# Kernel optimization log

Hardware: AMD Instinct MI355X
Metric: run time of the kernel (lower is better)

## Reference

```python
import jax, jax.numpy as jnp
import numpy as np

N = 100000
E = 1600000
IN = 128
H = 4
C = 32
NEG_SLOPE = 0.2


def setup_inputs() -> dict:
    key = jax.random.key(0)
    ks = jax.random.split(key, 10)
    feats = jax.random.normal(ks[0], (N, IN), dtype=jnp.float32)
    # edge_index with no self loops: dst = (src + offset) % N, offset in [1, N-1]
    src = jax.random.randint(ks[1], (E,), 0, N)
    off = jax.random.randint(ks[2], (E,), 1, N)
    dst = (src + off) % N
    edge_index = jnp.stack([src, dst]).astype(jnp.int64)
    scale = 1.0 / np.sqrt(IN)
    W_src = jax.random.uniform(ks[3], (H * C, IN), jnp.float32, -scale, scale)
    W_res = jax.random.uniform(ks[4], (H * C, IN), jnp.float32, -scale, scale)
    att_src = jax.random.normal(ks[5], (1, H, C), dtype=jnp.float32) * 0.1
    att_dst = jax.random.normal(ks[6], (1, H, C), dtype=jnp.float32) * 0.1
    bias = jnp.zeros((H * C,), dtype=jnp.float32)
    gamma = jnp.ones((H * C,), dtype=jnp.float32)
    beta = jnp.zeros((H * C,), dtype=jnp.float32)
    return {"feats": feats, "edge_index": edge_index, "W_src": W_src,
            "att_src": att_src, "att_dst": att_dst, "W_res": W_res,
            "bias": bias, "gamma": gamma, "beta": beta}


def reference(feats, edge_index, W_src, att_src, att_dst, W_res, bias, gamma, beta):
    n = feats.shape[0]
    # add self loops (edge_index has none by construction)
    loop = jnp.arange(n)
    src = jnp.concatenate([edge_index[0], loop])  # [E+N]
    dst = jnp.concatenate([edge_index[1], loop])
    xp = (feats @ W_src.T).reshape(n, H, C)          # [N,H,C]
    a_src = jnp.sum(xp * att_src, axis=-1)           # [N,H]
    a_dst = jnp.sum(xp * att_dst, axis=-1)           # [N,H]
    e = jax.nn.leaky_relu(a_src[src] + a_dst[dst], NEG_SLOPE)  # [E+N,H]
    # segment softmax over destination node
    m = jax.ops.segment_max(e, dst, num_segments=n)
    ex = jnp.exp(e - m[dst])
    s = jax.ops.segment_sum(ex, dst, num_segments=n)
    alpha = ex / (s[dst] + 1e-16)                    # [E+N,H]
    # weighted scatter-add aggregation
    msg = alpha[:, :, None] * xp[src]                # [E+N,H,C]
    out = jax.ops.segment_sum(msg, dst, num_segments=n)  # [N,H,C]
    res = (feats @ W_res.T).reshape(n, H, C)
    out = out + res + bias.reshape(1, H, C)
    out = out.reshape(n, H * C)                      # agg_modes='flatten'
    # BatchNorm1d, training mode (batch statistics, biased variance)
    mu = out.mean(axis=0)
    var = jnp.mean((out - mu) ** 2, axis=0)
    return (out - mu) / jnp.sqrt(var + 1e-5) * gamma + beta
```

## Files before the change

### kernel.cpp

```cpp
#include <hip/hip_runtime.h>
#include <hip/hip_fp16.h>

#define NEGS 0.2f
#define NB_AGGR 2048
#define NSHAD 16
#define NB_CSR 2048
#define CAP 64

typedef _Float16 f16x8 __attribute__((ext_vector_type(8)));
typedef float f32x2 __attribute__((ext_vector_type(2)));
typedef float f32x4 __attribute__((ext_vector_type(4)));

__device__ __forceinline__ float lrelu(float x){ return x > 0.f ? x : NEGS*x; }
__device__ __forceinline__ float sel4(float4 v, int h){
    float lo = (h & 1) ? v.y : v.x;
    float hi = (h & 1) ? v.w : v.z;
    return (h & 2) ? hi : lo;
}

__device__ __forceinline__ unsigned char f32_to_e4m3(float x){
    union { _Float16 f; unsigned short u; } c; c.f = (_Float16)x;
    unsigned u = c.u, s = (u >> 8) & 0x80, a = u & 0x7fff;
    if (a < 0x2400) return (unsigned char)s;
    a += 0x40;
    unsigned e = (a >> 10) - 8;
    unsigned m = (a >> 7) & 7;
    return (unsigned char)(s | (e << 3) | m);
}
template<bool HI>
__device__ __forceinline__ float2 fp8x2_to_f2(unsigned int packed){
#if __has_builtin(__builtin_amdgcn_cvt_pk_f32_fp8)
    f32x2 r = __builtin_amdgcn_cvt_pk_f32_fp8((int)packed, HI);
    return make_float2(r[0], r[1]);
#else
    unsigned short sv = HI ? (unsigned short)(packed >> 16) : (unsigned short)(packed & 0xffff);
    unsigned b0 = sv & 0xff, b1 = (sv >> 8) & 0xff;
    unsigned t0 = b0 & 0x7f, t1 = b1 & 0x7f;
    unsigned short u0 = (unsigned short)(((b0 & 0x80) << 8) | (t0 ? ((t0 + 64) << 7) : 0));
    unsigned short u1 = (unsigned short)(((b1 & 0x80) << 8) | (t1 ? ((t1 + 64) << 7) : 0));
    union { unsigned short u; _Float16 f; } c0, c1; c0.u = u0; c1.u = u1;
    return make_float2((float)c0.f, (float)c1.f);
#endif
}

__global__ __launch_bounds__(256) void k_wcvt(const float* __restrict__ Wsrc,
        const float* __restrict__ Wres, _Float16* __restrict__ WH){
    int t = blockIdx.x*256 + threadIdx.x;
    if (t < 16384)      WH[t] = (_Float16)Wsrc[t];
    else if (t < 32768) WH[t] = (_Float16)Wres[t - 16384];
}

__global__ __launch_bounds__(256, 3) void k_gemm(const float* __restrict__ feats,
        const _Float16* __restrict__ WH,
        const float* __restrict__ att_s, const float* __restrict__ att_d,
        unsigned char* __restrict__ xp8, float* __restrict__ res,
        float* __restrict__ a_src, float* __restrict__ a_dst, int n){
    __shared__ _Float16 As[8192];
    int t = threadIdx.x;
    int n0 = blockIdx.x * 64;
    const float4* f4 = (const float4*)feats;
    #pragma unroll
    for (int i = 0; i < 8; ++i){
        int idx = t + i*256;
        int row = idx >> 5, c4 = idx & 31;
        float4 v = make_float4(0.f,0.f,0.f,0.f);
        if (n0 + row < n) v = f4[(size_t)(n0+row)*32 + c4];
        int mt = row >> 4, l15r = row & 15;
        int kk = c4 >> 3, l4r = (c4 >> 1) & 3, jr = (c4 & 1)*4;
        int off = (mt*4 + kk)*512 + (l4r*16 + l15r)*8 + jr;
        As[off+0] = (_Float16)v.x; As[off+1] = (_Float16)v.y;
        As[off+2] = (_Float16)v.z; As[off+3] = (_Float16)v.w;
    }
    __syncthreads();
    int w = t >> 6, lane = t & 63;
    int l15 = lane & 15, l4 = lane >> 4;
    f32x4 acc[4][4];
    #pragma unroll
    for (int mt = 0; mt < 4; ++mt)
        #pragma unroll
        for (int nt = 0; nt < 4; ++nt)
            acc[mt][nt] = (f32x4){0.f,0.f,0.f,0.f};
    const f16x8* Bp = (const f16x8*)WH;
    #pragma unroll
    for (int kk = 0; kk < 4; ++kk){
        f16x8 a[4], b[4];
        #pragma unroll
        for (int mt = 0; mt < 4; ++mt)
            a[mt] = *(const f16x8*)&As[(mt*4 + kk)*512 + lane*8];
        #pragma unroll
        for (int nt = 0; nt < 4; ++nt){
            int col = w*64 + nt*16 + l15;
            b[nt] = Bp[col*16 + kk*4 + l4];
        }
        #pragma unroll
        for (int mt = 0; mt < 4; ++mt)
            #pragma unroll
            for (int nt = 0; nt < 4; ++nt)
                acc[mt][nt] = __builtin_amdgcn_mfma_f32_16x16x32_f16(a[mt], b[nt], acc[mt][nt], 0, 0, 0);
    }
    if (w < 2){
        float as0 = att_s[w*64 + l15],      as1 = att_s[w*64 + 16 + l15];
        float as2 = att_s[w*64 + 32 + l15], as3 = att_s[w*64 + 48 + l15];
        float ad0 = att_d[w*64 + l15],      ad1 = att_d[w*64 + 16 + l15];
        float ad2 = att_d[w*64 + 32 + l15], ad3 = att_d[w*64 + 48 + l15];
        #pragma unroll
        for (int mt = 0; mt < 4; ++mt){
            #pragma unroll
            for (int reg = 0; reg < 4; ++reg){
                int node = n0 + mt*16 + l4*4 + reg;
                float v0 = acc[mt][0][reg], v1 = acc[mt][1][reg];
                float v2 = acc[mt][2][reg], v3 = acc[mt][3][reg];
                if (node < n){
                    unsigned char* xp = xp8 + (size_t)node*128 + w*64 + l15;
                    xp[0]  = f32_to_e4m3(v0);
                    xp[16] = f32_to_e4m3(v1);
                    xp[32] = f32_to_e4m3(v2);
                    xp[48] = f32_to_e4m3(v3);
                }
                float ps0 = v0*as0 + v1*as1, ps1 = v2*as2 + v3*as3;
                float pd0 = v0*ad0 + v1*ad1, pd1 = v2*ad2 + v3*ad3;
                #pragma unroll
                for (int off = 1; off <= 8; off <<= 1){
                    ps0 += __shfl_xor(ps0, off); ps1 += __shfl_xor(ps1, off);
                    pd0 += __shfl_xor(pd0, off); pd1 += __shfl_xor(pd1, off);
                }
                if (l15 == 0 && node < n){
                    a_src[node*4 + 2*w]     = ps0;
                    a_src[node*4 + 2*w + 1] = ps1;
                    a_dst[node*4 + 2*w]     = pd0;
                    a_dst[node*4 + 2*w + 1] = pd1;
                }
            }
        }
    } else {
        int cbase = (w-2)*64;
        #pragma unroll
        for (int mt = 0; mt < 4; ++mt){
            #pragma unroll
            for (int reg = 0; reg < 4; ++reg){
                int node = n0 + mt*16 + l4*4 + reg;
                if (node < n){
                    float* rp = res + (size_t)node*128 + cbase + l15;
                    rp[0]  = acc[mt][0][reg];
                    rp[16] = acc[mt][1][reg];
                    rp[32] = acc[mt][2][reg];
                    rp[48] = acc[mt][3][reg];
                }
            }
        }
    }
}

__global__ __launch_bounds__(256) void k_scatter(const int* __restrict__ ei,
        int* __restrict__ cursor, int* __restrict__ nbr, int e, int n){
    int g  = blockIdx.x & 7;
    int bi = blockIdx.x >> 3;
    int chunk = (n + 7) >> 3;
    int lo = g*chunk, hi = min(n, lo + chunk);
    int tid = bi*256 + (int)threadIdx.x;
    const int4* d4 = (const int4*)(ei + e);
    int nv4 = e >> 2;
    const int stride = (NB_CSR/8)*256*2;
    for (int q = tid*2; q < nv4; q += stride){
        int4 a = d4[q];
        int4 b = (q+1 < nv4) ? d4[q+1] : make_int4(-1,-1,-1,-1);
        int ds[8] = {a.x, a.y, a.z, a.w, b.x, b.y, b.z, b.w};
        #pragma unroll
        for (int k = 0; k < 8; ++k){
            int d = ds[k];
            if (d >= lo && d < hi){
                int s = ei[q*4 + k];
                int pos = atomicAdd(&cursor[d], 1);
                if (pos < CAP) nbr[(size_t)d*CAP + pos] = s;
            }
        }
    }
    if (blockIdx.x == 0 && (int)threadIdx.x < (e & 3)){
        int i = (e & ~3) + (int)threadIdx.x;
        int d = ei[e + i];
        int s = ei[i];
        int pos = atomicAdd(&cursor[d], 1);
        if (pos < CAP) nbr[(size_t)d*CAP + pos] = s;
    }
}

__global__ __launch_bounds__(256, 4) void k_aggr(const unsigned char* __restrict__ xp8,
        const float* __restrict__ a_src, const float* __restrict__ a_dst,
        const int* __restrict__ cursor, const int* __restrict__ nbr,
        const float* __restrict__ bias, float* __restrict__ out,
        float* __restrict__ gshad, int n){
    __shared__ float lsum[4][128];
    __shared__ float lsq[4][128];
    __shared__ float wlds[4][32][4];
    int w = threadIdx.x >> 6, lane = threadIdx.x & 63;
    int sub = lane & 15;
    int e4  = lane >> 4;
    int h   = sub >> 2;
    const float4* a4 = (const float4*)a_src;
    const uint2* x8  = (const uint2*)xp8;
    float psum[8], psq[8];
    #pragma unroll
    for (int k = 0; k < 8; ++k){ psum[k]=0.f; psq[k]=0.f; }
    int ngroups = (n + 3) >> 2;
    for (int grp = blockIdx.x; grp < ngroups; grp += NB_AGGR){
        int node = grp*4 + w;
        if (node >= n) continue;
        float4 ad4 = *(const float4*)(a_dst + node*4);
        float adh = sel4(ad4, h);
        int deg = min(cursor[node], CAP);
        const int* nrow = nbr + (size_t)node*CAP;
        float acc[8];
        #pragma unroll
        for (int k = 0; k < 8; ++k) acc[k] = 0.f;
        float ssum = (e4 == 0) ? __expf(lrelu(a_src[node*4 + h] + adh)) : 0.f;
        float ws = ssum;
        uint2 xsraw = x8[(size_t)node*16 + sub];
        for (int ch0 = 0; ch0 < deg; ch0 += 32){
            int idx = ch0 + lane;
            if (idx > deg-1) idx = deg-1;
            int sidv = (lane < 32) ? nrow[idx] : node;
            float4 av = a4[sidv];
            if (lane < 32){
                float4 w4;
                w4.x = __expf(lrelu(av.x + ad4.x));
                w4.y = __expf(lrelu(av.y + ad4.y));
                w4.z = __expf(lrelu(av.z + ad4.z));
                w4.w = __expf(lrelu(av.w + ad4.w));
                *(float4*)&wlds[w][lane][0] = w4;
            }
            __builtin_amdgcn_wave_barrier();
            int sid[8];
            #pragma unroll
            for (int p = 0; p < 8; ++p) sid[p] = __shfl(sidv, p*4 + e4);
            uint2 xr[8];
            #pragma unroll
            for (int p = 0; p < 8; ++p) xr[p] = x8[(size_t)sid[p]*16 + sub];
            #pragma unroll
            for (int p = 0; p < 8; ++p){
                int j = p*4 + e4;
                float wgt = ((ch0 + j) < deg) ? wlds[w][j][h] : 0.f;
                ssum += wgt;
                float2 c0 = fp8x2_to_f2<false>(xr[p].x);
                float2 c1 = fp8x2_to_f2<true >(xr[p].x);
                float2 c2 = fp8x2_to_f2<false>(xr[p].y);
                float2 c3 = fp8x2_to_f2<true >(xr[p].y);
                acc[0] += wgt*c0.x; acc[1] += wgt*c0.y;
                acc[2] += wgt*c1.x; acc[3] += wgt*c1.y;
                acc[4] += wgt*c2.x; acc[5] += wgt*c2.y;
                acc[6] += wgt*c3.x; acc[7] += wgt*c3.y;
            }
        }
        #pragma unroll
        for (int off = 16; off <= 32; off <<= 1){
            #pragma unroll
            for (int k = 0; k < 8; ++k) acc[k] += __shfl_xor(acc[k], off);
            ssum += __shfl_xor(ssum, off);
        }
        float inv = 1.f/(ssum + 1e-16f);
        if (e4 == 0){
            float fs[8];
            float2 s0 = fp8x2_to_f2<false>(xsraw.x);
            float2 s1 = fp8x2_to_f2<true >(xsraw.x);
            float2 s2 = fp8x2_to_f2<false>(xsraw.y);
            float2 s3 = fp8x2_to_f2<true >(xsraw.y);
            fs[0]=s0.x; fs[1]=s0.y; fs[2]=s1.x; fs[3]=s1.y;
            fs[4]=s2.x; fs[5]=s2.y; fs[6]=s3.x; fs[7]=s3.y;
            float4 r0 = *(const float4*)(out + (size_t)node*128 + sub*8);
            float4 r1 = *(const float4*)(out + (size_t)node*128 + sub*8 + 4);
            float4 b0 = *(const float4*)(bias + sub*8);
            float4 b1 = *(const float4*)(bias + sub*8 + 4);
            float o[8];
            o[0] = (acc[0]+ws*fs[0])*inv + r0.x + b0.x; o[1] = (acc[1]+ws*fs[1])*inv + r0.y + b0.y;
            o[2] = (acc[2]+ws*fs[2])*inv + r0.z + b0.z; o[3] = (acc[3]+ws*fs[3])*inv + r0.w + b0.w;
            o[4] = (acc[4]+ws*fs[4])*inv + r1.x + b1.x; o[5] = (acc[5]+ws*fs[5])*inv + r1.y + b1.y;
            o[6] = (acc[6]+ws*fs[6])*inv + r1.z + b1.z; o[7] = (acc[7]+ws*fs[7])*inv + r1.w + b1.w;
            *(float4*)(out + (size_t)node*128 + sub*8)     = make_float4(o[0],o[1],o[2],o[3]);
            *(float4*)(out + (size_t)node*128 + sub*8 + 4) = make_float4(o[4],o[5],o[6],o[7]);
            #pragma unroll
            for (int k = 0; k < 8; ++k){ psum[k] += o[k]; psq[k] += o[k]*o[k]; }
        }
    }
    if (e4 == 0){
        *(float4*)&lsum[w][sub*8]   = make_float4(psum[0],psum[1],psum[2],psum[3]);
        *(float4*)&lsum[w][sub*8+4] = make_float4(psum[4],psum[5],psum[6],psum[7]);
        *(float4*)&lsq[w][sub*8]    = make_float4(psq[0],psq[1],psq[2],psq[3]);
        *(float4*)&lsq[w][sub*8+4]  = make_float4(psq[4],psq[5],psq[6],psq[7]);
    }
    __syncthreads();
    int t = threadIdx.x;
    float* shad = gshad + (blockIdx.x & (NSHAD-1))*256;
    if (t < 128){
        float s = lsum[0][t]+lsum[1][t]+lsum[2][t]+lsum[3][t];
        atomicAdd(&shad[t], s);
    } else {
        int c = t-128;
        float s = lsq[0][c]+lsq[1][c]+lsq[2][c]+lsq[3][c];
        atomicAdd(&shad[128 + c], s);
    }
}

__global__ void k_bnfin(const float* __restrict__ gshad,
        const float* __restrict__ gamma, const float* __restrict__ beta,
        float* __restrict__ scale, float* __restrict__ shift, int n){
    int t = threadIdx.x;
    if (t < 128){
        float s = 0.f, q = 0.f;
        #pragma unroll
        for (int c = 0; c < NSHAD; ++c){
            s += gshad[c*256 + t];
            q += gshad[c*256 + 128 + t];
        }
        float mu  = s/(float)n;
        float var = q/(float)n - mu*mu;
        float inv = rsqrtf(var + 1e-5f);
        float sc  = inv*gamma[t];
        scale[t] = sc;
        shift[t] = beta[t] - mu*sc;
    }
}

__global__ __launch_bounds__(256) void k_bnapply(float* __restrict__ out,
        const float* __restrict__ scale, const float* __restrict__ shift, long total4){
    __shared__ float sc[128], sh[128];
    if (threadIdx.x < 128){ sc[threadIdx.x]=scale[threadIdx.x]; sh[threadIdx.x]=shift[threadIdx.x]; }
    __syncthreads();
    long i = (long)blockIdx.x*blockDim.x + threadIdx.x;
    if (i < total4){
        float4* o4 = (float4*)out;
        float4 v = o4[i];
        int c = (int)((i & 31) * 4);
        v.x = v.x*sc[c+0]+sh[c+0];
        v.y = v.y*sc[c+1]+sh[c+1];
        v.z = v.z*sc[c+2]+sh[c+2];
        v.w = v.w*sc[c+3]+sh[c+3];
        o4[i]=v;
    }
}

extern "C" void kernel_launch(void* const* d_in, const int* in_sizes, int n_in,
                              void* d_out, int out_size, void* d_ws, size_t ws_size,
                              hipStream_t stream){
    const float* feats      = (const float*)d_in[0];
    const int* ei           = (const int*)d_in[1];
    const float* Wsrc       = (const float*)d_in[2];
    const float* att_s      = (const float*)d_in[3];
    const float* att_d      = (const float*)d_in[4];
    const float* Wres       = (const float*)d_in[5];
    const float* bias       = (const float*)d_in[6];
    const float* gamma      = (const float*)d_in[7];
    const float* beta       = (const float*)d_in[8];
    int n = in_sizes[0]/128;
    int e = in_sizes[1]/2;
    float* out = (float*)d_out;

    char* w = (char*)d_ws;
    unsigned char* xp8 = (unsigned char*)w; w += (size_t)n*128;
    float* a_src = (float*)w; w += (size_t)n*4*4;
    float* a_dst = (float*)w; w += (size_t)n*4*4;
    int*   cursor= (int*)w;   w += (size_t)n*4;
    int*   nbr   = (int*)w;   w += (size_t)n*CAP*4;
    float* gshad = (float*)w; w += (size_t)NSHAD*256*4;
    float* scale = (float*)w; w += 512;
    float* shift = (float*)w; w += 512;
    _Float16* WH = (_Float16*)w; w += 32768*2;

    hipMemsetAsync(cursor, 0, (size_t)n*4, stream);
    hipMemsetAsync(gshad,  0, (size_t)NSHAD*256*4, stream);

    k_wcvt<<<dim3(128), 256, 0, stream>>>(Wsrc, Wres, WH);
    k_gemm<<<dim3((n+63)/64), 256, 0, stream>>>(feats, WH, att_s, att_d, xp8, out, a_src, a_dst, n);
    k_scatter<<<dim3(NB_CSR), 256, 0, stream>>>(ei, cursor, nbr, e, n);
    k_aggr<<<dim3(NB_AGGR), 256, 0, stream>>>(xp8, a_src, a_dst, cursor, nbr, bias, out, gshad, n);
    k_bnfin<<<dim3(1), 128, 0, stream>>>(gshad, gamma, beta, scale, shift, n);
    long total4 = (long)n*32;
    k_bnapply<<<dim3((int)((total4+255)/256)), 256, 0, stream>>>(out, scale, shift, total4);
}
```

Baseline: 222.5 us.

## Co-schedule GEMM and CSR scatter in one launch; shrink aggregation chunk to 16

Merges the GEMM kernel and the edge-scatter (CSR build) kernel into a single launch, with odd blocks doing scatter and even blocks doing the GEMM. The two independent phases can then run concurrently on the GPU and one launch gap disappears. Separately, the aggregation loop now processes 16 neighbours per chunk instead of 32, so fewer lanes sit idle on low-degree nodes. The cost is fewer loads in flight per iteration and more loop trips for high-degree nodes. The fused kernel also carries the GEMM's shared memory and launch bounds on its scatter blocks, which may limit occupancy.

```diff
diff --git a/kernel.cpp b/kernel.cpp
--- a/kernel.cpp
+++ b/kernel.cpp
@@ -50,14 +50,53 @@
     else if (t < 32768) WH[t] = (_Float16)Wres[t - 16384];
 }
 
-__global__ __launch_bounds__(256, 3) void k_gemm(const float* __restrict__ feats,
+__global__ __launch_bounds__(256, 3) void k_gs(const float* __restrict__ feats,
         const _Float16* __restrict__ WH,
         const float* __restrict__ att_s, const float* __restrict__ att_d,
         unsigned char* __restrict__ xp8, float* __restrict__ res,
-        float* __restrict__ a_src, float* __restrict__ a_dst, int n){
+        float* __restrict__ a_src, float* __restrict__ a_dst, int n, int G_gemm,
+        const int* __restrict__ ei, int* __restrict__ cursor,
+        int* __restrict__ nbr, int e){
     __shared__ _Float16 As[8192];
+    int bx = blockIdx.x;
+    if (bx & 1){
+        int sid = bx >> 1;
+        if (sid >= NB_CSR) return;
+        int g  = sid & 7;
+        int bi = sid >> 3;
+        int chunk = (n + 7) >> 3;
+        int lo = g*chunk, hi = min(n, lo + chunk);
+        int tid = bi*256 + (int)threadIdx.x;
+        const int4* d4 = (const int4*)(ei + e);
+        int nv4 = e >> 2;
+        const int stride = (NB_CSR/8)*256*2;
+        for (int q = tid*2; q < nv4; q += stride){
+            int4 a = d4[q];
+            int4 b = (q+1 < nv4) ? d4[q+1] : make_int4(-1,-1,-1,-1);
+            int ds[8] = {a.x, a.y, a.z, a.w, b.x, b.y, b.z, b.w};
+            #pragma unroll
+            for (int k = 0; k < 8; ++k){
+                int d = ds[k];
+                if (d >= lo && d < hi){
+                    int s = ei[q*4 + k];
+                    int pos = atomicAdd(&cursor[d], 1);
+                    if (pos < CAP) nbr[(size_t)d*CAP + pos] = s;
+                }
+            }
+        }
+        if (sid == 0 && (int)threadIdx.x < (e & 3)){
+            int i = (e & ~3) + (int)threadIdx.x;
+            int d = ei[e + i];
+            int s = ei[i];
+            int pos = atomicAdd(&cursor[d], 1);
+            if (pos < CAP) nbr[(size_t)d*CAP + pos] = s;
+        }
+        return;
+    }
+    int gid = bx >> 1;
+    if (gid >= G_gemm) return;
     int t = threadIdx.x;
-    int n0 = blockIdx.x * 64;
+    int n0 = gid * 64;
     const float4* f4 = (const float4*)feats;
     #pragma unroll
     for (int i = 0; i < 8; ++i){
@@ -151,39 +190,6 @@
     }
 }
 
-__global__ __launch_bounds__(256) void k_scatter(const int* __restrict__ ei,
-        int* __restrict__ cursor, int* __restrict__ nbr, int e, int n){
-    int g  = blockIdx.x & 7;
-    int bi = blockIdx.x >> 3;
-    int chunk = (n + 7) >> 3;
-    int lo = g*chunk, hi = min(n, lo + chunk);
-    int tid = bi*256 + (int)threadIdx.x;
-    const int4* d4 = (const int4*)(ei + e);
-    int nv4 = e >> 2;
-    const int stride = (NB_CSR/8)*256*2;
-    for (int q = tid*2; q < nv4; q += stride){
-        int4 a = d4[q];
-        int4 b = (q+1 < nv4) ? d4[q+1] : make_int4(-1,-1,-1,-1);
-        int ds[8] = {a.x, a.y, a.z, a.w, b.x, b.y, b.z, b.w};
-        #pragma unroll
-        for (int k = 0; k < 8; ++k){
-            int d = ds[k];
-            if (d >= lo && d < hi){
-                int s = ei[q*4 + k];
-                int pos = atomicAdd(&cursor[d], 1);
-                if (pos < CAP) nbr[(size_t)d*CAP + pos] = s;
-            }
-        }
-    }
-    if (blockIdx.x == 0 && (int)threadIdx.x < (e & 3)){
-        int i = (e & ~3) + (int)threadIdx.x;
-        int d = ei[e + i];
-        int s = ei[i];
-        int pos = atomicAdd(&cursor[d], 1);
-        if (pos < CAP) nbr[(size_t)d*CAP + pos] = s;
-    }
-}
-
 __global__ __launch_bounds__(256, 4) void k_aggr(const unsigned char* __restrict__ xp8,
         const float* __restrict__ a_src, const float* __restrict__ a_dst,
         const int* __restrict__ cursor, const int* __restrict__ nbr,
@@ -191,7 +197,7 @@
         float* __restrict__ gshad, int n){
     __shared__ float lsum[4][128];
     __shared__ float lsq[4][128];
-    __shared__ float wlds[4][32][4];
+    __shared__ float wlds[4][16][4];
     int w = threadIdx.x >> 6, lane = threadIdx.x & 63;
     int sub = lane & 15;
     int e4  = lane >> 4;
@@ -215,12 +221,13 @@
         float ssum = (e4 == 0) ? __expf(lrelu(a_src[node*4 + h] + adh)) : 0.f;
         float ws = ssum;
         uint2 xsraw = x8[(size_t)node*16 + sub];
-        for (int ch0 = 0; ch0 < deg; ch0 += 32){
-            int idx = ch0 + lane;
-            if (idx > deg-1) idx = deg-1;
-            int sidv = (lane < 32) ? nrow[idx] : node;
-            float4 av = a4[sidv];
-            if (lane < 32){
+        for (int ch0 = 0; ch0 < deg; ch0 += 16){
+            int sidv = node;
+            if (lane < 16){
+                int idx = ch0 + lane;
+                if (idx > deg-1) idx = deg-1;
+                sidv = nrow[idx];
+                float4 av = a4[sidv];
                 float4 w4;
                 w4.x = __expf(lrelu(av.x + ad4.x));
                 w4.y = __expf(lrelu(av.y + ad4.y));
@@ -229,14 +236,14 @@
                 *(float4*)&wlds[w][lane][0] = w4;
             }
             __builtin_amdgcn_wave_barrier();
-            int sid[8];
-            #pragma unroll
-            for (int p = 0; p < 8; ++p) sid[p] = __shfl(sidv, p*4 + e4);
-            uint2 xr[8];
-            #pragma unroll
-            for (int p = 0; p < 8; ++p) xr[p] = x8[(size_t)sid[p]*16 + sub];
-            #pragma unroll
-            for (int p = 0; p < 8; ++p){
+            int sid[4];
+            #pragma unroll
+            for (int p = 0; p < 4; ++p) sid[p] = __shfl(sidv, p*4 + e4);
+            uint2 xr[4];
+            #pragma unroll
+            for (int p = 0; p < 4; ++p) xr[p] = x8[(size_t)sid[p]*16 + sub];
+            #pragma unroll
+            for (int p = 0; p < 4; ++p){
                 int j = p*4 + e4;
                 float wgt = ((ch0 + j) < deg) ? wlds[w][j][h] : 0.f;
                 ssum += wgt;
@@ -367,9 +374,11 @@
     hipMemsetAsync(cursor, 0, (size_t)n*4, stream);
     hipMemsetAsync(gshad,  0, (size_t)NSHAD*256*4, stream);
 
+    int G_gemm = (n + 63) / 64;
+    int grid_gs = 2 * ((G_gemm > NB_CSR) ? G_gemm : NB_CSR);
     k_wcvt<<<dim3(128), 256, 0, stream>>>(Wsrc, Wres, WH);
-    k_gemm<<<dim3((n+63)/64), 256, 0, stream>>>(feats, WH, att_s, att_d, xp8, out, a_src, a_dst, n);
-    k_scatter<<<dim3(NB_CSR), 256, 0, stream>>>(ei, cursor, nbr, e, n);
+    k_gs<<<dim3(grid_gs), 256, 0, stream>>>(feats, WH, att_s, att_d, xp8, out, a_src, a_dst, n, G_gemm,
+                                            ei, cursor, nbr, e);
     k_aggr<<<dim3(NB_AGGR), 256, 0, stream>>>(xp8, a_src, a_dst, cursor, nbr, bias, out, gshad, n);
     k_bnfin<<<dim3(1), 128, 0, stream>>>(gshad, gamma, beta, scale, shift, n);
     long total4 = (long)n*32;
```

Result: slower. 228.2 us (+2.6%).
